# Optimization experiments

Measured on AMD Instinct MI355X. Metric: run time of the kernel, lower is better.

## Reference

```python
import jax, jax.numpy as jnp
import numpy as np

NUM_HEADS = 8


def _conv1x1(x, W, b):
    # 1x1 conv == per-pixel linear: x [N,C,H,W], W [O,C], b [O]
    return jnp.einsum('nchw,oc->nohw', x, W) + b[None, :, None, None]


def setup_inputs() -> dict:
    key = jax.random.key(0)
    ks = jax.random.split(key, 10)
    C = 512
    s = 1.0 / np.sqrt(C)  # keep pre-softmax logits in a sane range
    return {
        'x': jax.random.normal(ks[0], (2, C, 64, 64), dtype=jnp.float32),
        'Wq': jax.random.normal(ks[1], (C, C), dtype=jnp.float32) * s,
        'bq': jax.random.normal(ks[2], (C,), dtype=jnp.float32) * 0.01,
        'Wk': jax.random.normal(ks[3], (C, C), dtype=jnp.float32) * s,
        'bk': jax.random.normal(ks[4], (C,), dtype=jnp.float32) * 0.01,
        'Wv': jax.random.normal(ks[5], (C, C), dtype=jnp.float32) * s,
        'bv': jax.random.normal(ks[6], (C,), dtype=jnp.float32) * 0.01,
        'Wo': jax.random.normal(ks[7], (C, C), dtype=jnp.float32) * s,
        'bo': jax.random.normal(ks[8], (C,), dtype=jnp.float32) * 0.01,
        'gamma': jax.random.normal(ks[9], (1,), dtype=jnp.float32),
    }


def reference(x, Wq, bq, Wk, bk, Wv, bv, Wo, bo, gamma):
    N, C, H, W = x.shape
    nh = NUM_HEADS
    hd = C // nh
    S = H * W
    scale = 1.0 / (hd ** 0.5)
    # Projections via 1x1 conv, then split heads over flattened spatial tokens
    Q = _conv1x1(x, Wq, bq).reshape(N, nh, hd, S).transpose(0, 1, 3, 2)  # [N,h,S,d]
    K = _conv1x1(x, Wk, bk).reshape(N, nh, hd, S)                         # [N,h,d,S]
    V = _conv1x1(x, Wv, bv).reshape(N, nh, hd, S).transpose(0, 1, 3, 2)  # [N,h,S,d]
    attn = jax.nn.softmax(jnp.einsum('nhsd,nhdt->nhst', Q, K) * scale, axis=-1)
    out = jnp.einsum('nhst,nhtd->nhsd', attn, V)                          # [N,h,S,d]
    out = out.transpose(0, 1, 3, 2).reshape(N, C, H, W)
    out = _conv1x1(out, Wo, bo)
    return gamma[0] * out + x
```

## Files before the change

kernel.cpp:

```cpp
#include <hip/hip_runtime.h>
#include <hip/hip_bf16.h>

typedef __attribute__((ext_vector_type(4))) float f32x4;
typedef __attribute__((ext_vector_type(16))) float f32x16;
typedef __attribute__((ext_vector_type(8))) short s16x8;
typedef __attribute__((ext_vector_type(4))) unsigned short us16x4;
typedef __attribute__((ext_vector_type(4))) unsigned int u32x4;

#define C_DIM 512
#define S_DIM 4096
#define NB 2
#define NH 8
#define HD 64

#define QSCALE 0.1803368801111244f

__device__ __forceinline__ unsigned short f2bf(float f) {
    union { float f; unsigned u; } v; v.f = f;
    unsigned r = v.u + 0x7FFFu + ((v.u >> 16) & 1u);
    return (unsigned short)(r >> 16);
}

__device__ __forceinline__ float dev_exp2(float x) {
    float r;
    asm("v_exp_f32 %0, %1" : "=v"(r) : "v"(x));
    return r;
}

__device__ __forceinline__ unsigned cvt_pk_bf16(float lo, float hi) {
    unsigned r;
    asm("v_cvt_pk_bf16_f32 %0, %1, %2" : "=v"(r) : "v"(lo), "v"(hi));
    return r;
}

__device__ __forceinline__ void lane_swap(unsigned& a, unsigned& b) {
    asm("v_permlane32_swap_b32 %0, %1" : "+v"(a), "+v"(b));
}
__device__ __forceinline__ void lane_swapf(float& a, float& b) {
    asm("v_permlane32_swap_b32 %0, %1" : "+v"(a), "+v"(b));
}

__device__ __forceinline__ void gload_lds16(const void* g, void* l) {
    __builtin_amdgcn_global_load_lds(
        (const __attribute__((address_space(1))) void*)g,
        (__attribute__((address_space(3))) void*)l, 16, 0, 0);
}

__global__ __launch_bounds__(256) void wconv_kernel(
    const float* __restrict__ Wq, const float* __restrict__ Wk,
    const float* __restrict__ Wv, const float* __restrict__ Wo,
    unsigned short* __restrict__ Wb) {
    int i = blockIdx.x * 256 + threadIdx.x;
    int y = blockIdx.y;
    const float* src = (y == 0) ? Wq : (y == 1) ? Wk : (y == 2) ? Wv : Wo;
    Wb[(size_t)y * 262144 + i] = f2bf(src[i]);
}

__global__ __launch_bounds__(256) void xpose_kernel(
    const float* __restrict__ x, unsigned short* __restrict__ Xt) {
    __shared__ float tile[32][33];
    int n = blockIdx.z;
    int s0 = blockIdx.x * 32;
    int c0 = blockIdx.y * 32;
    int tx = threadIdx.x & 31;
    int ty = threadIdx.x >> 5;
#pragma unroll
    for (int r = 0; r < 4; ++r) {
        int c = c0 + ty + r * 8;
        tile[ty + r * 8][tx] = x[((size_t)n * C_DIM + c) * S_DIM + s0 + tx];
    }
    __syncthreads();
#pragma unroll
    for (int r = 0; r < 4; ++r) {
        int s = s0 + ty + r * 8;
        Xt[((size_t)n * S_DIM + s) * C_DIM + c0 + tx] = f2bf(tile[tx][ty + r * 8]);
    }
}

__global__ __launch_bounds__(256) void qkv_gemm_kernel(
    const unsigned short* __restrict__ Wb, const unsigned short* __restrict__ Xt,
    const float* __restrict__ bq, const float* __restrict__ bk, const float* __restrict__ bv,
    unsigned short* __restrict__ Qt, unsigned short* __restrict__ Kt,
    unsigned short* __restrict__ Vb) {
    __shared__ unsigned short As[128 * 64];
    __shared__ unsigned short Bs[128 * 64];
    int w = blockIdx.z >> 1;
    int n = blockIdx.z & 1;
    const unsigned short* A = Wb + (size_t)w * 262144;
    const unsigned short* B = Xt + (size_t)n * S_DIM * C_DIM;
    int tid = threadIdx.x;
    int wid = tid >> 6, lane = tid & 63;
    int wm = wid >> 1, wn = wid & 1;
    int lr = lane & 15, lq = lane >> 4;
    int bm = blockIdx.y * 128, bt = blockIdx.x * 128;
    int r_in = lane >> 3, c8 = (lane & 7) * 8;

    f32x4 zero = {0.f, 0.f, 0.f, 0.f};
    f32x4 acc[4][4];
#pragma unroll
    for (int i = 0; i < 4; ++i)
#pragma unroll
        for (int j = 0; j < 4; ++j) acc[i][j] = zero;

    for (int ks = 0; ks < 8; ++ks) {
#pragma unroll
        for (int q = 0; q < 4; ++q) {
            int row = wid * 32 + q * 8;
            gload_lds16(A + (size_t)(bm + row + r_in) * C_DIM + ks * 64 + c8, &As[row * 64]);
            gload_lds16(B + (size_t)(bt + row + r_in) * C_DIM + ks * 64 + c8, &Bs[row * 64]);
        }
        __syncthreads();
#pragma unroll
        for (int kk = 0; kk < 2; ++kk) {
            s16x8 af[4], bf[4];
#pragma unroll
            for (int i = 0; i < 4; ++i)
                af[i] = *(const s16x8*)&As[(wm * 64 + i * 16 + lr) * 64 + kk * 32 + lq * 8];
#pragma unroll
            for (int j = 0; j < 4; ++j)
                bf[j] = *(const s16x8*)&Bs[(wn * 64 + j * 16 + lr) * 64 + kk * 32 + lq * 8];
#pragma unroll
            for (int i = 0; i < 4; ++i)
#pragma unroll
                for (int j = 0; j < 4; ++j)
                    acc[i][j] = __builtin_amdgcn_mfma_f32_16x16x32_bf16(af[i], bf[j], acc[i][j], 0, 0, 0);
        }
        __syncthreads();
    }

    const float* bias = (w == 0) ? bq : (w == 1) ? bk : bv;
#pragma unroll
    for (int i = 0; i < 4; ++i) {
        int obase = bm + wm * 64 + i * 16 + lq * 4;
#pragma unroll
        for (int j = 0; j < 4; ++j) {
            int t = bt + wn * 64 + j * 16 + lr;
            if (w == 0) {
                us16x4 pk;
#pragma unroll
                for (int r = 0; r < 4; ++r)
                    pk[r] = f2bf((acc[i][j][r] + bias[obase + r]) * QSCALE);
                int h = obase >> 6, d = obase & 63;
                *(us16x4*)&Qt[(((size_t)(n * NH + h) * S_DIM) + t) * HD + d] = pk;
            } else if (w == 1) {
                us16x4 pk;
#pragma unroll
                for (int r = 0; r < 4; ++r) pk[r] = f2bf(acc[i][j][r] + bias[obase + r]);
                int h = obase >> 6, d = obase & 63;
                *(us16x4*)&Kt[(((size_t)(n * NH + h) * S_DIM) + t) * HD + d] = pk;
            } else {
#pragma unroll
                for (int r = 0; r < 4; ++r) {
                    int o = obase + r;
                    Vb[((size_t)(n * C_DIM + o)) * S_DIM + t] = f2bf(acc[i][j][r] + bias[o]);
                }
            }
        }
    }
}

__global__ __launch_bounds__(256, 1) void attn_kernel(
    const unsigned short* __restrict__ Qt, const unsigned short* __restrict__ Kt,
    const unsigned short* __restrict__ Vb, unsigned short* __restrict__ Ot) {
    __shared__ unsigned short Ks[2][64 * 64];
    __shared__ unsigned short Vs[2][64 * 64];
    int tid = threadIdx.x, wid = tid >> 6, lane = tid & 63;
    int l31 = lane & 31, hi = lane >> 5;
    int sw = l31 & 7;

    int bidl = blockIdx.x;
    int swz = (bidl & 7) * 32 + (bidl >> 3);
    int nh = swz >> 4;
    int qb = swz & 15;
    int n = nh >> 3, h = nh & 7;
    int qrow0 = qb * 256 + wid * 64;

    const unsigned short* Qh = Qt + (size_t)nh * S_DIM * HD;
    const unsigned short* Kh = Kt + (size_t)nh * S_DIM * HD;
    const unsigned short* Vh = Vb + ((size_t)(n * C_DIM + h * HD)) * S_DIM;

    s16x8 qf[2][4];
#pragma unroll
    for (int qs = 0; qs < 2; ++qs)
#pragma unroll
        for (int st = 0; st < 4; ++st)
            qf[qs][st] = *(const s16x8*)&Qh[((size_t)(qrow0 + qs * 32 + l31)) * HD + st * 16 + hi * 8];

    f32x16 Oacc[2][2];
#pragma unroll
    for (int qs = 0; qs < 2; ++qs)
#pragma unroll
        for (int jm = 0; jm < 2; ++jm)
#pragma unroll
            for (int r = 0; r < 16; ++r) Oacc[qs][jm][r] = 0.f;
    float l_run[2] = {0.f, 0.f};

    int srow0 = tid >> 3, sslot = tid & 7;
    int ws0 = (sslot ^ (srow0 & 7)) * 8;

    s16x8 kreg[2], vreg[2];
#pragma unroll
    for (int q = 0; q < 2; ++q) {
        int row = srow0 + q * 32;
        kreg[q] = *(const s16x8*)&Kh[((size_t)row) * HD + sslot * 8];
        vreg[q] = *(const s16x8*)&Vh[((size_t)row) * S_DIM + sslot * 8];
    }
#pragma unroll
    for (int q = 0; q < 2; ++q) {
        int row = srow0 + q * 32;
        *(s16x8*)&Ks[0][row * 64 + ws0] = kreg[q];
        *(s16x8*)&Vs[0][row * 64 + ws0] = vreg[q];
    }
    __syncthreads();

    for (int kt = 0; kt < 64; ++kt) {
        int cur = kt & 1;
        if (kt < 63) {
#pragma unroll
            for (int q = 0; q < 2; ++q) {
                int row = srow0 + q * 32;
                kreg[q] = *(const s16x8*)&Kh[((size_t)((kt + 1) * 64 + row)) * HD + sslot * 8];
                vreg[q] = *(const s16x8*)&Vh[((size_t)row) * S_DIM + (kt + 1) * 64 + sslot * 8];
            }
        }

        f32x16 s_[2][2];
#pragma unroll
        for (int qs = 0; qs < 2; ++qs)
#pragma unroll
            for (int jm = 0; jm < 2; ++jm)
#pragma unroll
                for (int r = 0; r < 16; ++r) s_[qs][jm][r] = 0.f;
#pragma unroll
        for (int st = 0; st < 4; ++st) {
            int slot = ((2 * st + hi) ^ sw) * 8;
            s16x8 kf0 = *(const s16x8*)&Ks[cur][l31 * 64 + slot];
            s16x8 kf1 = *(const s16x8*)&Ks[cur][(32 + l31) * 64 + slot];
            s_[0][0] = __builtin_amdgcn_mfma_f32_32x32x16_bf16(kf0, qf[0][st], s_[0][0], 0, 0, 0);
            s_[1][0] = __builtin_amdgcn_mfma_f32_32x32x16_bf16(kf0, qf[1][st], s_[1][0], 0, 0, 0);
            s_[0][1] = __builtin_amdgcn_mfma_f32_32x32x16_bf16(kf1, qf[0][st], s_[0][1], 0, 0, 0);
            s_[1][1] = __builtin_amdgcn_mfma_f32_32x32x16_bf16(kf1, qf[1][st], s_[1][1], 0, 0, 0);
        }

        s16x8 pf[2][4];
#pragma unroll
        for (int qs = 0; qs < 2; ++qs) {
            float rs = 0.f;
#pragma unroll
            for (int jm = 0; jm < 2; ++jm) {
                float p[16];
#pragma unroll
                for (int r = 0; r < 16; ++r) { p[r] = dev_exp2(s_[qs][jm][r]); rs += p[r]; }
                unsigned pk0 = cvt_pk_bf16(p[0],  p[1]);
                unsigned pk1 = cvt_pk_bf16(p[2],  p[3]);
                unsigned pk2 = cvt_pk_bf16(p[4],  p[5]);
                unsigned pk3 = cvt_pk_bf16(p[6],  p[7]);
                unsigned pk4 = cvt_pk_bf16(p[8],  p[9]);
                unsigned pk5 = cvt_pk_bf16(p[10], p[11]);
                unsigned pk6 = cvt_pk_bf16(p[12], p[13]);
                unsigned pk7 = cvt_pk_bf16(p[14], p[15]);
                lane_swap(pk2, pk0);
                lane_swap(pk3, pk1);
                lane_swap(pk6, pk4);
                lane_swap(pk7, pk5);
                u32x4 w0 = {pk0, pk1, pk2, pk3};
                u32x4 w1 = {pk4, pk5, pk6, pk7};
                pf[qs][2 * jm]     = __builtin_bit_cast(s16x8, w0);
                pf[qs][2 * jm + 1] = __builtin_bit_cast(s16x8, w1);
            }
            l_run[qs] += rs;
        }

#pragma unroll
        for (int kk = 0; kk < 4; ++kk) {
            int slot = ((kk * 2 + hi) ^ sw) * 8;
            s16x8 vf0 = *(const s16x8*)&Vs[cur][l31 * 64 + slot];
            s16x8 vf1 = *(const s16x8*)&Vs[cur][(32 + l31) * 64 + slot];
            Oacc[0][0] = __builtin_amdgcn_mfma_f32_32x32x16_bf16(vf0, pf[0][kk], Oacc[0][0], 0, 0, 0);
            Oacc[1][0] = __builtin_amdgcn_mfma_f32_32x32x16_bf16(vf0, pf[1][kk], Oacc[1][0], 0, 0, 0);
            Oacc[0][1] = __builtin_amdgcn_mfma_f32_32x32x16_bf16(vf1, pf[0][kk], Oacc[0][1], 0, 0, 0);
            Oacc[1][1] = __builtin_amdgcn_mfma_f32_32x32x16_bf16(vf1, pf[1][kk], Oacc[1][1], 0, 0, 0);
        }

        if (kt < 63) {
            int nxt = cur ^ 1;
#pragma unroll
            for (int q = 0; q < 2; ++q) {
                int row = srow0 + q * 32;
                *(s16x8*)&Ks[nxt][row * 64 + ws0] = kreg[q];
                *(s16x8*)&Vs[nxt][row * 64 + ws0] = vreg[q];
            }
            __syncthreads();
        }
    }

#pragma unroll
    for (int qs = 0; qs < 2; ++qs) {
        float a = l_run[qs], b = l_run[qs];
        lane_swapf(a, b);
        float inv = 1.f / (a + b);
        int token = qrow0 + qs * 32 + l31;
        unsigned short* orow = Ot + ((size_t)n * S_DIM + token) * C_DIM + h * HD;
#pragma unroll
        for (int jm2 = 0; jm2 < 2; ++jm2)
#pragma unroll
            for (int rq = 0; rq < 4; ++rq) {
                int d = jm2 * 32 + 8 * rq + 4 * hi;
                us16x4 pk;
#pragma unroll
                for (int r = 0; r < 4; ++r) pk[r] = f2bf(Oacc[qs][jm2][rq * 4 + r] * inv);
                *(us16x4*)&orow[d] = pk;
            }
    }
}

__global__ __launch_bounds__(256) void out_gemm_kernel(
    const unsigned short* __restrict__ Wb, const unsigned short* __restrict__ Ot,
    const float* __restrict__ bo, const float* __restrict__ gamma,
    const float* __restrict__ xin, float* __restrict__ out) {
    __shared__ unsigned short As[128 * 64];
    __shared__ unsigned short Bs[128 * 64];
    int n = blockIdx.z;
    const unsigned short* A = Wb + (size_t)3 * 262144;
    const unsigned short* B = Ot + (size_t)n * S_DIM * C_DIM;
    int tid = threadIdx.x;
    int wid = tid >> 6, lane = tid & 63;
    int wm = wid >> 1, wn = wid & 1;
    int lr = lane & 15, lq = lane >> 4;
    int bm = blockIdx.y * 128, bt = blockIdx.x * 128;
    int r_in = lane >> 3, c8 = (lane & 7) * 8;

    f32x4 zero = {0.f, 0.f, 0.f, 0.f};
    f32x4 acc[4][4];
#pragma unroll
    for (int i = 0; i < 4; ++i)
#pragma unroll
        for (int j = 0; j < 4; ++j) acc[i][j] = zero;

    for (int ks = 0; ks < 8; ++ks) {
#pragma unroll
        for (int q = 0; q < 4; ++q) {
            int row = wid * 32 + q * 8;
            gload_lds16(A + (size_t)(bm + row + r_in) * C_DIM + ks * 64 + c8, &As[row * 64]);
            gload_lds16(B + (size_t)(bt + row + r_in) * C_DIM + ks * 64 + c8, &Bs[row * 64]);
        }
        __syncthreads();
#pragma unroll
        for (int kk = 0; kk < 2; ++kk) {
            s16x8 af[4], bf[4];
#pragma unroll
            for (int i = 0; i < 4; ++i)
                af[i] = *(const s16x8*)&As[(wm * 64 + i * 16 + lr) * 64 + kk * 32 + lq * 8];
#pragma unroll
            for (int j = 0; j < 4; ++j)
                bf[j] = *(const s16x8*)&Bs[(wn * 64 + j * 16 + lr) * 64 + kk * 32 + lq * 8];
#pragma unroll
            for (int i = 0; i < 4; ++i)
#pragma unroll
                for (int j = 0; j < 4; ++j)
                    acc[i][j] = __builtin_amdgcn_mfma_f32_16x16x32_bf16(af[i], bf[j], acc[i][j], 0, 0, 0);
        }
        __syncthreads();
    }

    float g = gamma[0];
#pragma unroll
    for (int i = 0; i < 4; ++i) {
        int obase = bm + wm * 64 + i * 16 + lq * 4;
#pragma unroll
        for (int j = 0; j < 4; ++j) {
            int t = bt + wn * 64 + j * 16 + lr;
#pragma unroll
            for (int r = 0; r < 4; ++r) {
                int o = obase + r;
                size_t idx = ((size_t)(n * C_DIM + o)) * S_DIM + t;
                out[idx] = g * (acc[i][j][r] + bo[o]) + xin[idx];
            }
        }
    }
}

extern "C" void kernel_launch(void* const* d_in, const int* in_sizes, int n_in,
                              void* d_out, int out_size, void* d_ws, size_t ws_size,
                              hipStream_t stream) {
    const float* x  = (const float*)d_in[0];
    const float* Wq = (const float*)d_in[1];
    const float* bq = (const float*)d_in[2];
    const float* Wk = (const float*)d_in[3];
    const float* bk = (const float*)d_in[4];
    const float* Wv = (const float*)d_in[5];
    const float* bv = (const float*)d_in[6];
    const float* Wo = (const float*)d_in[7];
    const float* bo = (const float*)d_in[8];
    const float* gamma = (const float*)d_in[9];
    float* out = (float*)d_out;

    char* ws = (char*)d_ws;
    unsigned short* Wb = (unsigned short*)ws;
    unsigned short* Xt = (unsigned short*)(ws + ((size_t)2  << 20));
    unsigned short* Qt = (unsigned short*)(ws + ((size_t)10 << 20));
    unsigned short* Kt = (unsigned short*)(ws + ((size_t)18 << 20));
    unsigned short* Vb = (unsigned short*)(ws + ((size_t)26 << 20));
    unsigned short* Ot = (unsigned short*)(ws + ((size_t)34 << 20));

    wconv_kernel<<<dim3(1024, 4), 256, 0, stream>>>(Wq, Wk, Wv, Wo, Wb);
    xpose_kernel<<<dim3(128, 16, 2), 256, 0, stream>>>(x, Xt);
    qkv_gemm_kernel<<<dim3(32, 4, 6), 256, 0, stream>>>(Wb, Xt, bq, bk, bv, Qt, Kt, Vb);
    attn_kernel<<<256, 256, 0, stream>>>(Qt, Kt, Vb, Ot);
    out_gemm_kernel<<<dim3(32, 4, 2), 256, 0, stream>>>(Wb, Ot, bo, gamma, x, out);
}
```

Measured before the change: 155.5 us.

## Split attention KV range in two and merge partials in a combine kernel

The attention kernel now splits each query block's key/value range into two halves, launching twice as many blocks. Each block writes unnormalized bf16 partial outputs and fp32 row sums, and a new combine kernel adds the halves and normalizes. This lets 512 blocks fill an MI355X with 256 CUs more fully than 256 blocks did, and the launch-bounds occupancy hint is relaxed. In exchange it adds a partial-output round trip through memory, an extra launch, and bf16 rounding of the partials. The LDS swizzle is also changed to XOR in higher row bits.

```diff
diff --git a/kernel.cpp b/kernel.cpp
--- a/kernel.cpp
+++ b/kernel.cpp
@@ -19,6 +19,11 @@
     union { float f; unsigned u; } v; v.f = f;
     unsigned r = v.u + 0x7FFFu + ((v.u >> 16) & 1u);
     return (unsigned short)(r >> 16);
+}
+
+__device__ __forceinline__ float bf2f(unsigned short u) {
+    union { unsigned u; float f; } v; v.u = ((unsigned)u) << 16;
+    return v.f;
 }
 
 __device__ __forceinline__ float dev_exp2(float x) {
@@ -159,21 +164,25 @@
     }
 }
 
-__global__ __launch_bounds__(256, 1) void attn_kernel(
+__global__ __launch_bounds__(256) void attn_kernel(
     const unsigned short* __restrict__ Qt, const unsigned short* __restrict__ Kt,
-    const unsigned short* __restrict__ Vb, unsigned short* __restrict__ Ot) {
+    const unsigned short* __restrict__ Vb, unsigned short* __restrict__ Opart,
+    float* __restrict__ Lpart) {
     __shared__ unsigned short Ks[2][64 * 64];
     __shared__ unsigned short Vs[2][64 * 64];
     int tid = threadIdx.x, wid = tid >> 6, lane = tid & 63;
     int l31 = lane & 31, hi = lane >> 5;
-    int sw = l31 & 7;
+    int radj = (l31 & 7) ^ ((l31 >> 3) & 3);
 
     int bidl = blockIdx.x;
-    int swz = (bidl & 7) * 32 + (bidl >> 3);
-    int nh = swz >> 4;
-    int qb = swz & 15;
+    int swz = (bidl & 7) * 64 + (bidl >> 3);
+    int nh = swz >> 5;
+    int rem = swz & 31;
+    int qb = rem >> 1;
+    int half = rem & 1;
     int n = nh >> 3, h = nh & 7;
     int qrow0 = qb * 256 + wid * 64;
+    int kvbase = half * 2048;
 
     const unsigned short* Qh = Qt + (size_t)nh * S_DIM * HD;
     const unsigned short* Kh = Kt + (size_t)nh * S_DIM * HD;
@@ -196,31 +205,31 @@
     float l_run[2] = {0.f, 0.f};
 
     int srow0 = tid >> 3, sslot = tid & 7;
-    int ws0 = (sslot ^ (srow0 & 7)) * 8;
+    int wslot = (sslot ^ (srow0 & 7) ^ ((srow0 >> 3) & 3)) * 8;
 
     s16x8 kreg[2], vreg[2];
 #pragma unroll
     for (int q = 0; q < 2; ++q) {
         int row = srow0 + q * 32;
-        kreg[q] = *(const s16x8*)&Kh[((size_t)row) * HD + sslot * 8];
-        vreg[q] = *(const s16x8*)&Vh[((size_t)row) * S_DIM + sslot * 8];
+        kreg[q] = *(const s16x8*)&Kh[((size_t)(kvbase + row)) * HD + sslot * 8];
+        vreg[q] = *(const s16x8*)&Vh[((size_t)row) * S_DIM + kvbase + sslot * 8];
     }
 #pragma unroll
     for (int q = 0; q < 2; ++q) {
         int row = srow0 + q * 32;
-        *(s16x8*)&Ks[0][row * 64 + ws0] = kreg[q];
-        *(s16x8*)&Vs[0][row * 64 + ws0] = vreg[q];
+        *(s16x8*)&Ks[0][row * 64 + wslot] = kreg[q];
+        *(s16x8*)&Vs[0][row * 64 + wslot] = vreg[q];
     }
     __syncthreads();
 
-    for (int kt = 0; kt < 64; ++kt) {
+    for (int kt = 0; kt < 32; ++kt) {
         int cur = kt & 1;
-        if (kt < 63) {
+        if (kt < 31) {
 #pragma unroll
             for (int q = 0; q < 2; ++q) {
                 int row = srow0 + q * 32;
-                kreg[q] = *(const s16x8*)&Kh[((size_t)((kt + 1) * 64 + row)) * HD + sslot * 8];
-                vreg[q] = *(const s16x8*)&Vh[((size_t)row) * S_DIM + (kt + 1) * 64 + sslot * 8];
+                kreg[q] = *(const s16x8*)&Kh[((size_t)(kvbase + (kt + 1) * 64 + row)) * HD + sslot * 8];
+                vreg[q] = *(const s16x8*)&Vh[((size_t)row) * S_DIM + kvbase + (kt + 1) * 64 + sslot * 8];
             }
         }
 
@@ -233,7 +242,7 @@
                 for (int r = 0; r < 16; ++r) s_[qs][jm][r] = 0.f;
 #pragma unroll
         for (int st = 0; st < 4; ++st) {
-            int slot = ((2 * st + hi) ^ sw) * 8;
+            int slot = ((2 * st + hi) ^ radj) * 8;
             s16x8 kf0 = *(const s16x8*)&Ks[cur][l31 * 64 + slot];
             s16x8 kf1 = *(const s16x8*)&Ks[cur][(32 + l31) * 64 + slot];
             s_[0][0] = __builtin_amdgcn_mfma_f32_32x32x16_bf16(kf0, qf[0][st], s_[0][0], 0, 0, 0);
@@ -273,7 +282,7 @@
 
 #pragma unroll
         for (int kk = 0; kk < 4; ++kk) {
-            int slot = ((kk * 2 + hi) ^ sw) * 8;
+            int slot = ((kk * 2 + hi) ^ radj) * 8;
             s16x8 vf0 = *(const s16x8*)&Vs[cur][l31 * 64 + slot];
             s16x8 vf1 = *(const s16x8*)&Vs[cur][(32 + l31) * 64 + slot];
             Oacc[0][0] = __builtin_amdgcn_mfma_f32_32x32x16_bf16(vf0, pf[0][kk], Oacc[0][0], 0, 0, 0);
@@ -282,13 +291,13 @@
             Oacc[1][1] = __builtin_amdgcn_mfma_f32_32x32x16_bf16(vf1, pf[1][kk], Oacc[1][1], 0, 0, 0);
         }
 
-        if (kt < 63) {
+        if (kt < 31) {
             int nxt = cur ^ 1;
 #pragma unroll
             for (int q = 0; q < 2; ++q) {
                 int row = srow0 + q * 32;
-                *(s16x8*)&Ks[nxt][row * 64 + ws0] = kreg[q];
-                *(s16x8*)&Vs[nxt][row * 64 + ws0] = vreg[q];
+                *(s16x8*)&Ks[nxt][row * 64 + wslot] = kreg[q];
+                *(s16x8*)&Vs[nxt][row * 64 + wslot] = vreg[q];
             }
             __syncthreads();
         }
@@ -296,11 +305,8 @@
 
 #pragma unroll
     for (int qs = 0; qs < 2; ++qs) {
-        float a = l_run[qs], b = l_run[qs];
-        lane_swapf(a, b);
-        float inv = 1.f / (a + b);
         int token = qrow0 + qs * 32 + l31;
-        unsigned short* orow = Ot + ((size_t)n * S_DIM + token) * C_DIM + h * HD;
+        unsigned short* obase = Opart + (((size_t)(half * 16 + nh) * S_DIM + token) * HD);
 #pragma unroll
         for (int jm2 = 0; jm2 < 2; ++jm2)
 #pragma unroll
@@ -308,10 +314,35 @@
                 int d = jm2 * 32 + 8 * rq + 4 * hi;
                 us16x4 pk;
 #pragma unroll
-                for (int r = 0; r < 4; ++r) pk[r] = f2bf(Oacc[qs][jm2][rq * 4 + r] * inv);
-                *(us16x4*)&orow[d] = pk;
-            }
-    }
+                for (int r = 0; r < 4; ++r) pk[r] = f2bf(Oacc[qs][jm2][rq * 4 + r]);
+                *(us16x4*)&obase[d] = pk;
+            }
+        float a = l_run[qs], b = l_run[qs];
+        lane_swapf(a, b);
+        float tot = a + b;
+        if (hi == 0)
+            Lpart[(size_t)(half * 16 + nh) * S_DIM + token] = tot;
+    }
+}
+
+__global__ __launch_bounds__(256) void combine_kernel(
+    const unsigned short* __restrict__ Opart, const float* __restrict__ Lpart,
+    unsigned short* __restrict__ Ot) {
+    int g = blockIdx.x * 256 + threadIdx.x;
+    int d4 = (g & 15) * 4;
+    int s = (g >> 4) & 4095;
+    int nh = g >> 16;
+    size_t base0 = ((size_t)nh * S_DIM + s) * HD + d4;
+    size_t base1 = base0 + (size_t)16 * S_DIM * HD;
+    us16x4 o0 = *(const us16x4*)&Opart[base0];
+    us16x4 o1 = *(const us16x4*)&Opart[base1];
+    float l = Lpart[(size_t)nh * S_DIM + s] + Lpart[(size_t)(16 + nh) * S_DIM + s];
+    float inv = 1.f / l;
+    int n = nh >> 3, h = nh & 7;
+    us16x4 pk;
+#pragma unroll
+    for (int r = 0; r < 4; ++r) pk[r] = f2bf((bf2f(o0[r]) + bf2f(o1[r])) * inv);
+    *(us16x4*)&Ot[((size_t)n * S_DIM + s) * C_DIM + h * HD + d4] = pk;
 }
 
 __global__ __launch_bounds__(256) void out_gemm_kernel(
@@ -402,10 +433,13 @@
     unsigned short* Kt = (unsigned short*)(ws + ((size_t)18 << 20));
     unsigned short* Vb = (unsigned short*)(ws + ((size_t)26 << 20));
     unsigned short* Ot = (unsigned short*)(ws + ((size_t)34 << 20));
+    unsigned short* Opart = (unsigned short*)(ws + ((size_t)42 << 20));
+    float* Lpart = (float*)(ws + ((size_t)60 << 20));
 
     wconv_kernel<<<dim3(1024, 4), 256, 0, stream>>>(Wq, Wk, Wv, Wo, Wb);
     xpose_kernel<<<dim3(128, 16, 2), 256, 0, stream>>>(x, Xt);
     qkv_gemm_kernel<<<dim3(32, 4, 6), 256, 0, stream>>>(Wb, Xt, bq, bk, bv, Qt, Kt, Vb);
-    attn_kernel<<<256, 256, 0, stream>>>(Qt, Kt, Vb, Ot);
+    attn_kernel<<<512, 256, 0, stream>>>(Qt, Kt, Vb, Opart, Lpart);
+    combine_kernel<<<4096, 256, 0, stream>>>(Opart, Lpart, Ot);
     out_gemm_kernel<<<dim3(32, 4, 2), 256, 0, stream>>>(Wb, Ot, bo, gamma, x, out);
 }
```

Measured after the change: 153.5 us. Within noise of the previous version (-1.3%).
